# Optimization experiments

Hardware: AMD Instinct MI355X
Metric: run time of the kernel (lower is better)

Reference implementation:

```python
import jax, jax.numpy as jnp
import numpy as np

B, S, CC, CF, E, H, NH = 16, 1024, 8, 8, 64, 1024, 16
DH = H // NH
VOCAB = 10000
EPS = 1e-5


def layer_norm(x, g, b):
    m = x.mean(-1, keepdims=True)
    v = x.var(-1, keepdims=True)
    return (x - m) / jnp.sqrt(v + EPS) * g + b


def setup_inputs():
    key = jax.random.key(0)
    ks = jax.random.split(key, 30)
    f32 = jnp.float32
    n = lambda k, shp, s=0.02: jax.random.normal(k, shp, f32) * s
    inp = {}
    inp['cate_x'] = jax.random.randint(ks[0], (B, S, CC), 0, VOCAB)
    inp['cont_x'] = jax.random.normal(ks[1], (B, S, CF), f32)
    inp['mask'] = jax.random.randint(ks[2], (B, S), 0, 2)
    # parameters
    inp['emb_table'] = n(ks[3], (VOCAB, E)).at[0].set(0.0)  # padding_idx=0
    inp['cate_W'] = n(ks[4], (CC * E, H)); inp['cate_b'] = jnp.zeros((H,), f32)
    inp['cate_ln_g'] = jnp.ones((H,), f32); inp['cate_ln_b'] = jnp.zeros((H,), f32)
    inp['bn_g'] = jnp.ones((CF,), f32); inp['bn_b'] = jnp.zeros((CF,), f32)
    inp['cont_W'] = n(ks[5], (CF, H)); inp['cont_b'] = jnp.zeros((H,), f32)
    inp['cont_ln_g'] = jnp.ones((H,), f32); inp['cont_ln_b'] = jnp.zeros((H,), f32)
    inp['comb_W'] = n(ks[6], (2 * H, H)); inp['comb_b'] = jnp.zeros((H,), f32)
    inp['comb_ln_g'] = jnp.ones((H,), f32); inp['comb_ln_b'] = jnp.zeros((H,), f32)
    inp['Wq'] = n(ks[7], (H, H)); inp['bq'] = jnp.zeros((H,), f32)
    inp['Wk'] = n(ks[8], (H, H)); inp['bk'] = jnp.zeros((H,), f32)
    inp['Wv'] = n(ks[9], (H, H)); inp['bv'] = jnp.zeros((H,), f32)
    inp['Wo'] = n(ks[10], (H, H)); inp['bo'] = jnp.zeros((H,), f32)
    return inp


def reference(cate_x, cont_x, mask, emb_table, cate_W, cate_b, cate_ln_g, cate_ln_b,
              bn_g, bn_b, cont_W, cont_b, cont_ln_g, cont_ln_b,
              comb_W, comb_b, comb_ln_g, comb_ln_b,
              Wq, bq, Wk, bk, Wv, bv, Wo, bo):
    # categorical path: embed -> flatten cols -> Linear+LN
    cate_emb = emb_table[cate_x].reshape(B, S, CC * E)
    cate_h = layer_norm(cate_emb @ cate_W + cate_b, cate_ln_g, cate_ln_b)
    # continuous path: BatchNorm1d over flattened (B*S, CF) with batch stats
    xf = cont_x.reshape(-1, CF)
    mu = xf.mean(0)
    var = xf.var(0)  # biased, as torch BN normalization
    xn = ((xf - mu) / jnp.sqrt(var + EPS) * bn_g + bn_b).reshape(B, S, CF)
    cont_h = layer_norm(xn @ cont_W + cont_b, cont_ln_g, cont_ln_b)
    # combine: ReLU -> Linear -> LN
    seq = jax.nn.relu(jnp.concatenate([cate_h, cont_h], axis=2))
    x = layer_norm(seq @ comb_W + comb_b, comb_ln_g, comb_ln_b)  # [B,S,H]
    # multi-head attention (dropout is identity in eval)
    Q = (x @ Wq + bq).reshape(B, S, NH, DH)
    K = (x @ Wk + bk).reshape(B, S, NH, DH)
    V = (x @ Wv + bv).reshape(B, S, NH, DH)
    scores = jnp.einsum('bqhd,bkhd->bhqk', Q, K) / np.sqrt(DH).astype(np.float32)
    # faithful to source: mask broadcast over the QUERY axis
    scores = jnp.where(mask[:, None, :, None] == 0, -1e7, scores)
    attn = jax.nn.softmax(scores, axis=-1)
    out = jnp.einsum('bhqk,bkhd->bqhd', attn, V).reshape(B, S, H)
    out = out @ Wo + bo
    return out[:, -1:, -1]  # [B,1]
```

## Files before the change

### kernel.cpp

```cpp
#include <hip/hip_runtime.h>
#include <hip/hip_bf16.h>
#include <math.h>

#define EPS 1e-5f

typedef unsigned short u16;
typedef __attribute__((ext_vector_type(8))) short bf16x8;
typedef __attribute__((ext_vector_type(4))) float f32x4;

__device__ __forceinline__ float b2f(u16 u) {
  union { unsigned int i; float f; } v; v.i = ((unsigned int)u) << 16; return v.f;
}
__device__ __forceinline__ u16 f2b(float f) {
  union { float f; unsigned int i; } v; v.f = f;
  unsigned int r = v.i + 0x7fff + ((v.i >> 16) & 1);
  return (u16)(r >> 16);
}

__device__ __forceinline__ void gload_lds16(const u16* g, u16* l) {
  __builtin_amdgcn_global_load_lds(
      (const __attribute__((address_space(1))) unsigned int*)g,
      (__attribute__((address_space(3))) unsigned int*)l, 16, 0, 0);
}

__global__ __launch_bounds__(256) void prep_k(
    const float* __restrict__ cx, float* __restrict__ part_bn,
    float* __restrict__ outacc,
    const float* __restrict__ emb, u16* __restrict__ embb,
    const float* __restrict__ cate_W, u16* __restrict__ cateWT,
    const float* __restrict__ comb_W, u16* __restrict__ combWT,
    const float* __restrict__ Wv, const float* __restrict__ Wo,
    float* __restrict__ wvo) {
  __shared__ float shmem[64 * 65];
  const int bid = blockIdx.x, tid = threadIdx.x;

  if (bid == 0) {
    if (tid < 16) outacc[tid] = 0.f;
    return;
  }
  if (bid <= 64) {
    int pb = bid - 1;
    int gid = pb * 256 + tid;
    float4 a = ((const float4*)cx)[2 * gid];
    float4 b = ((const float4*)cx)[2 * gid + 1];
    float v[16];
    v[0] = a.x; v[1] = a.y; v[2] = a.z; v[3] = a.w;
    v[4] = b.x; v[5] = b.y; v[6] = b.z; v[7] = b.w;
#pragma unroll
    for (int i = 0; i < 8; ++i) v[8 + i] = v[i] * v[i];
#pragma unroll
    for (int off = 32; off; off >>= 1)
#pragma unroll
      for (int i = 0; i < 16; ++i) v[i] += __shfl_down(v[i], off);
    int l = tid & 63, wv_ = tid >> 6;
    if (l == 0)
#pragma unroll
      for (int i = 0; i < 16; ++i) shmem[wv_ * 16 + i] = v[i];
    __syncthreads();
    if (tid < 16)
      part_bn[pb * 16 + tid] = shmem[tid] + shmem[16 + tid] + shmem[32 + tid] + shmem[48 + tid];
    return;
  }
  if (bid <= 689) {
    int i = (bid - 65) * 256 + tid;
    if (i < 160000) {
      float4 v = ((const float4*)emb)[i];
      ushort4 u; u.x = f2b(v.x); u.y = f2b(v.y); u.z = f2b(v.z); u.w = f2b(v.w);
      ((ushort4*)embb)[i] = u;
    }
    return;
  }
  if (bid <= 1329) {
    const float* W; u16* WT; int K, local;
    if (bid <= 817) { W = cate_W; WT = cateWT; K = 512;  local = bid - 690; }
    else            { W = comb_W; WT = combWT; K = 2048; local = bid - 818; }
    int n0 = (local & 15) * 64, k0 = (local >> 4) * 64;
    int c = tid & 63, r0 = tid >> 6;
#pragma unroll
    for (int i = 0; i < 16; ++i) {
      int r = r0 + i * 4;
      shmem[r * 65 + c] = W[(size_t)(k0 + r) * 1024 + n0 + c];
    }
    __syncthreads();
#pragma unroll
    for (int i = 0; i < 16; ++i) {
      int r = r0 + i * 4;
      WT[(size_t)(n0 + r) * K + k0 + c] = f2b(shmem[c * 65 + r]);
    }
    return;
  }
  {
    int local = bid - 1330;
    int h = local >> 2, jc = local & 3;
    if (tid < 64) shmem[tid] = Wo[(size_t)(h * 64 + tid) * 1024 + 1023];
    __syncthreads();
    int j = jc * 256 + tid;
    const float* vr = Wv + (size_t)j * 1024 + h * 64;
    float s = 0.f;
    for (int d4 = 0; d4 < 64; d4 += 4) {
      float4 w4 = *(const float4*)(vr + d4);
      s = fmaf(w4.x, shmem[d4], s);
      s = fmaf(w4.y, shmem[d4 + 1], s);
      s = fmaf(w4.z, shmem[d4 + 2], s);
      s = fmaf(w4.w, shmem[d4 + 3], s);
    }
    wvo[h * 1024 + j] = s;
  }
}

template <int MODE>
__global__ __launch_bounds__(512) void gemm256(
    const u16* __restrict__ A0, const u16* __restrict__ A1,
    const int* __restrict__ idx, const u16* __restrict__ embb,
    const u16* __restrict__ BT, const float* __restrict__ bias,
    u16* __restrict__ C, int K) {
  __shared__ u16 As[2][2][8192];
  __shared__ u16 Bs[2][2][8192];
  const int tid = threadIdx.x;
  const int bid = blockIdx.x;
  const int chunk = gridDim.x >> 3;
  const int swz = (bid & 7) * chunk + (bid >> 3);
  const int row0 = (swz >> 2) * 256;
  const int col0 = (swz & 3) * 256;

  const int rr8 = tid >> 3;
  const int p8  = tid & 7;
  const int sl  = p8 ^ (rr8 & 7);

  const int l   = tid & 63;
  const int w   = tid >> 6;
  const int wrh = w >> 2;
  const int wcq = w & 3;
  const int hb  = wcq >> 1;
  const int rbb = (wcq & 1) * 64;
  const int lr  = l & 15;
  const int lk  = l >> 4;

  f32x4 acc[8][4];
#pragma unroll
  for (int m = 0; m < 8; ++m)
#pragma unroll
    for (int n = 0; n < 4; ++n) acc[m][n] = (f32x4){0.f, 0.f, 0.f, 0.f};

  const int nt = K >> 6;
  const int nit = nt >> 1;

  auto stageA = [&](int t, int h) {
    const int k0 = t << 6;
    const int buf = t & 1;
#pragma unroll
    for (int i = 0; i < 2; ++i) {
      int ar = row0 + h * 128 + i * 64 + rr8;
      const u16* asrc;
      if (MODE == 1) {
        int id = idx[ar * 8 + (k0 >> 6)];
        asrc = embb + (size_t)id * 64 + sl * 8;
      } else {
        const u16* base = (k0 < 1024) ? A0 : A1;
        asrc = base + (size_t)ar * 1024 + (k0 & 1023) + sl * 8;
      }
      gload_lds16(asrc, &As[buf][h][i * 4096 + tid * 8]);
    }
  };
  auto stageB = [&](int t, int h) {
    const int k0 = t << 6;
    const int buf = t & 1;
#pragma unroll
    for (int i = 0; i < 2; ++i) {
      int br = col0 + h * 128 + i * 64 + rr8;
      gload_lds16(BT + (size_t)br * K + k0 + sl * 8,
                  &Bs[buf][h][i * 4096 + tid * 8]);
    }
  };

  bf16x8 bfr[4][2];
  auto loadB = [&](int buf) {
#pragma unroll
    for (int n = 0; n < 4; ++n)
#pragma unroll
      for (int ks = 0; ks < 2; ++ks) {
        int rowb = rbb + n * 16 + lr;
        int ph = (ks * 4 + lk) ^ (lr & 7);
        bfr[n][ks] = *(const bf16x8*)&Bs[buf][hb][rowb * 64 + ph * 8];
      }
  };
  auto loadA = [&](bf16x8 (&af)[2][2], int buf, int q) {
#pragma unroll
    for (int mm = 0; mm < 2; ++mm)
#pragma unroll
      for (int ks = 0; ks < 2; ++ks) {
        int rowa = (q * 2 + mm) * 16 + lr;
        int ph = (ks * 4 + lk) ^ (lr & 7);
        af[mm][ks] = *(const bf16x8*)&As[buf][wrh][rowa * 64 + ph * 8];
      }
  };
  auto mfma_quad = [&](bf16x8 (&af)[2][2], int q) {
    __builtin_amdgcn_s_setprio(1);
#pragma unroll
    for (int ks = 0; ks < 2; ++ks)
#pragma unroll
      for (int mm = 0; mm < 2; ++mm)
#pragma unroll
        for (int n = 0; n < 4; ++n)
          acc[q * 2 + mm][n] = __builtin_amdgcn_mfma_f32_16x16x32_bf16(
              af[mm][ks], bfr[n][ks], acc[q * 2 + mm][n], 0, 0, 0);
    __builtin_amdgcn_s_setprio(0);
  };

  stageA(0, 0); stageA(0, 1);
  stageB(0, 0); stageB(0, 1);
  stageB(1, 0); stageB(1, 1);
  asm volatile("s_waitcnt vmcnt(4)" ::: "memory");
  __builtin_amdgcn_s_barrier();

  for (int it = 0; it < nit; ++it) {
    const int T = it * 2;
    const bool more = (T + 2 < nt);
    bf16x8 af[2][2];

    loadB(0); loadA(af, 0, 0);
    stageA(T + 1, 0);
    __builtin_amdgcn_s_barrier();
    asm volatile("s_waitcnt lgkmcnt(0)" ::: "memory");
    mfma_quad(af, 0);
    __builtin_amdgcn_s_barrier();
    loadA(af, 0, 1);
    stageA(T + 1, 1);
    __builtin_amdgcn_s_barrier();
    asm volatile("s_waitcnt lgkmcnt(0)" ::: "memory");
    mfma_quad(af, 1);
    __builtin_amdgcn_s_barrier();
    loadA(af, 0, 2);
    if (more) stageB(T + 2, 0);
    __builtin_amdgcn_s_barrier();
    asm volatile("s_waitcnt lgkmcnt(0)" ::: "memory");
    mfma_quad(af, 2);
    __builtin_amdgcn_s_barrier();
    loadA(af, 0, 3);
    if (more) stageB(T + 2, 1);
    __builtin_amdgcn_s_barrier();
    asm volatile("s_waitcnt lgkmcnt(0)" ::: "memory");
    mfma_quad(af, 3);
    if (more) asm volatile("s_waitcnt vmcnt(4)" ::: "memory");
    else      asm volatile("s_waitcnt vmcnt(0)" ::: "memory");
    __builtin_amdgcn_s_barrier();

    loadB(1); loadA(af, 1, 0);
    if (more) stageA(T + 2, 0);
    __builtin_amdgcn_s_barrier();
    asm volatile("s_waitcnt lgkmcnt(0)" ::: "memory");
    mfma_quad(af, 0);
    __builtin_amdgcn_s_barrier();
    loadA(af, 1, 1);
    if (more) stageA(T + 2, 1);
    __builtin_amdgcn_s_barrier();
    asm volatile("s_waitcnt lgkmcnt(0)" ::: "memory");
    mfma_quad(af, 1);
    __builtin_amdgcn_s_barrier();
    loadA(af, 1, 2);
    if (more) stageB(T + 3, 0);
    __builtin_amdgcn_s_barrier();
    asm volatile("s_waitcnt lgkmcnt(0)" ::: "memory");
    mfma_quad(af, 2);
    __builtin_amdgcn_s_barrier();
    loadA(af, 1, 3);
    if (more) stageB(T + 3, 1);
    __builtin_amdgcn_s_barrier();
    asm volatile("s_waitcnt lgkmcnt(0)" ::: "memory");
    mfma_quad(af, 3);
    if (it + 1 < nit) {
      asm volatile("s_waitcnt vmcnt(4)" ::: "memory");
      __builtin_amdgcn_s_barrier();
    }
  }

  float bv_[4];
#pragma unroll
  for (int n = 0; n < 4; ++n) bv_[n] = bias[col0 + wcq * 64 + n * 16 + lr];
#pragma unroll
  for (int m = 0; m < 8; ++m) {
#pragma unroll
    for (int n = 0; n < 4; ++n) {
      int cc = col0 + wcq * 64 + n * 16 + lr;
#pragma unroll
      for (int q4 = 0; q4 < 4; ++q4) {
        int rr = row0 + wrh * 128 + m * 16 + lk * 4 + q4;
        C[(size_t)rr * 1024 + cc] = f2b(acc[m][n][q4] + bv_[n]);
      }
    }
  }
}

__global__ __launch_bounds__(256) void ln_k(u16* __restrict__ buf,
                                            const float* __restrict__ g,
                                            const float* __restrict__ b, int relu) {
  int lane = threadIdx.x & 63, wave = threadIdx.x >> 6;
  size_t row = (size_t)blockIdx.x * 4 + wave;
  u16* p = buf + row * 1024 + lane * 16;
  uint4 u0 = *(uint4*)p;
  uint4 u1 = *(uint4*)(p + 8);
  float x[16];
#pragma unroll
  for (int i = 0; i < 4; ++i) {
    unsigned int w0 = ((unsigned int*)&u0)[i];
    unsigned int w1 = ((unsigned int*)&u1)[i];
    x[2 * i]     = b2f((u16)(w0 & 0xffff));
    x[2 * i + 1] = b2f((u16)(w0 >> 16));
    x[8 + 2 * i]     = b2f((u16)(w1 & 0xffff));
    x[8 + 2 * i + 1] = b2f((u16)(w1 >> 16));
  }
  float s = 0.f, s2 = 0.f;
#pragma unroll
  for (int i = 0; i < 16; ++i) { s += x[i]; s2 += x[i] * x[i]; }
#pragma unroll
  for (int off = 32; off; off >>= 1) { s += __shfl_xor(s, off); s2 += __shfl_xor(s2, off); }
  float mean = s * (1.f / 1024.f);
  float var = s2 * (1.f / 1024.f) - mean * mean;
  float rs = rsqrtf(var + EPS);
  float y[16];
#pragma unroll
  for (int q = 0; q < 4; ++q) {
    float4 gv = *(const float4*)(g + lane * 16 + q * 4);
    float4 bv = *(const float4*)(b + lane * 16 + q * 4);
    y[4 * q]     = (x[4 * q]     - mean) * rs * gv.x + bv.x;
    y[4 * q + 1] = (x[4 * q + 1] - mean) * rs * gv.y + bv.y;
    y[4 * q + 2] = (x[4 * q + 2] - mean) * rs * gv.z + bv.z;
    y[4 * q + 3] = (x[4 * q + 3] - mean) * rs * gv.w + bv.w;
  }
  if (relu)
#pragma unroll
    for (int i = 0; i < 16; ++i) y[i] = fmaxf(y[i], 0.f);
  uint4 o0, o1;
#pragma unroll
  for (int i = 0; i < 4; ++i) {
    ((unsigned int*)&o0)[i] = (unsigned int)f2b(y[2 * i]) | ((unsigned int)f2b(y[2 * i + 1]) << 16);
    ((unsigned int*)&o1)[i] = (unsigned int)f2b(y[8 + 2 * i]) | ((unsigned int)f2b(y[8 + 2 * i + 1]) << 16);
  }
  *(uint4*)p = o0;
  *(uint4*)(p + 8) = o1;
}

__global__ __launch_bounds__(256) void cont_k(const float* __restrict__ cx,
                                              const float* __restrict__ part_bn,
                                              const float* __restrict__ bn_g,
                                              const float* __restrict__ bn_b,
                                              const float* __restrict__ W,
                                              const float* __restrict__ cb,
                                              const float* __restrict__ g,
                                              const float* __restrict__ bb,
                                              u16* __restrict__ out) {
  int row0 = blockIdx.x * 8, tid = threadIdx.x;
  __shared__ float sp[4][16];
  __shared__ float tt[16];
  __shared__ float ab[2][8];
  __shared__ float xn[8][8];
  __shared__ float rr1[4][8], rr2[4][8];

  if (tid < 64) {
    int f = tid & 15, qd = tid >> 4;
    float s = 0.f;
    for (int j = qd * 16; j < qd * 16 + 16; ++j) s += part_bn[j * 16 + f];
    sp[qd][f] = s;
  }
  __syncthreads();
  if (tid < 16) tt[tid] = sp[0][tid] + sp[1][tid] + sp[2][tid] + sp[3][tid];
  __syncthreads();
  if (tid < 8) {
    float mu = tt[tid] * (1.f / 16384.f);
    float var = tt[8 + tid] * (1.f / 16384.f) - mu * mu;
    float a = rsqrtf(var + EPS) * bn_g[tid];
    ab[0][tid] = a;
    ab[1][tid] = bn_b[tid] - mu * a;
  }
  __syncthreads();
  if (tid < 64) {
    int r = tid >> 3, f = tid & 7;
    xn[r][f] = ab[0][f] * cx[(row0 + r) * 8 + f] + ab[1][f];
  }
  __syncthreads();

  int c = tid * 4;
  float4 cbv = *(const float4*)(cb + c);
  float acc[8][4];
#pragma unroll
  for (int r = 0; r < 8; ++r) {
    acc[r][0] = cbv.x; acc[r][1] = cbv.y; acc[r][2] = cbv.z; acc[r][3] = cbv.w;
  }
  for (int k = 0; k < 8; ++k) {
    float4 w4 = *(const float4*)(W + k * 1024 + c);
#pragma unroll
    for (int r = 0; r < 8; ++r) {
      float xv = xn[r][k];
      acc[r][0] = fmaf(xv, w4.x, acc[r][0]);
      acc[r][1] = fmaf(xv, w4.y, acc[r][1]);
      acc[r][2] = fmaf(xv, w4.z, acc[r][2]);
      acc[r][3] = fmaf(xv, w4.w, acc[r][3]);
    }
  }
  float s1[8], s2[8];
#pragma unroll
  for (int r = 0; r < 8; ++r) {
    s1[r] = acc[r][0] + acc[r][1] + acc[r][2] + acc[r][3];
    s2[r] = acc[r][0] * acc[r][0] + acc[r][1] * acc[r][1] +
            acc[r][2] * acc[r][2] + acc[r][3] * acc[r][3];
  }
#pragma unroll
  for (int off = 32; off; off >>= 1)
#pragma unroll
    for (int r = 0; r < 8; ++r) {
      s1[r] += __shfl_down(s1[r], off);
      s2[r] += __shfl_down(s2[r], off);
    }
  int lane = tid & 63, wv = tid >> 6;
  if (lane == 0)
#pragma unroll
    for (int r = 0; r < 8; ++r) { rr1[wv][r] = s1[r]; rr2[wv][r] = s2[r]; }
  __syncthreads();
  float4 gv = *(const float4*)(g + c);
  float4 bv = *(const float4*)(bb + c);
#pragma unroll
  for (int r = 0; r < 8; ++r) {
    float ss = rr1[0][r] + rr1[1][r] + rr1[2][r] + rr1[3][r];
    float qq = rr2[0][r] + rr2[1][r] + rr2[2][r] + rr2[3][r];
    float mean = ss * (1.f / 1024.f);
    float var = qq * (1.f / 1024.f) - mean * mean;
    float rs = rsqrtf(var + EPS);
    float y0 = fmaxf((acc[r][0] - mean) * rs * gv.x + bv.x, 0.f);
    float y1 = fmaxf((acc[r][1] - mean) * rs * gv.y + bv.y, 0.f);
    float y2 = fmaxf((acc[r][2] - mean) * rs * gv.z + bv.z, 0.f);
    float y3 = fmaxf((acc[r][3] - mean) * rs * gv.w + bv.w, 0.f);
    ushort4 o; o.x = f2b(y0); o.y = f2b(y1); o.z = f2b(y2); o.w = f2b(y3);
    *(ushort4*)(out + (size_t)(row0 + r) * 1024 + c) = o;
  }
}

__global__ __launch_bounds__(256) void qproj_k(const u16* __restrict__ x,
                                               const float* __restrict__ Wq,
                                               const float* __restrict__ bq,
                                               float* __restrict__ q) {
  __shared__ u16 xs[16][1024];
  __shared__ float part[16][16][16];
  int tid = threadIdx.x;
  for (int i = tid; i < 4096; i += 256) {
    int b = i >> 8, off = (i & 255) * 4;
    *(ushort4*)&xs[b][off] =
        *(const ushort4*)(x + ((size_t)(b * 1024 + 1023)) * 1024 + off);
  }
  __syncthreads();
  int c = tid & 15;
  int col = blockIdx.x * 16 + c;
  int kq = tid >> 4;
  float acc[16];
#pragma unroll
  for (int b = 0; b < 16; ++b) acc[b] = 0.f;
  for (int k = kq * 64; k < kq * 64 + 64; ++k) {
    float wv = Wq[(size_t)k * 1024 + col];
#pragma unroll
    for (int b = 0; b < 16; ++b) acc[b] = fmaf(b2f(xs[b][k]), wv, acc[b]);
  }
#pragma unroll
  for (int b = 0; b < 16; ++b) part[kq][b][c] = acc[b];
  __syncthreads();
  if (tid < 256) {
    int b = tid >> 4, cc = tid & 15;
    float s = 0.f;
#pragma unroll
    for (int j = 0; j < 16; ++j) s += part[j][b][cc];
    q[b * 1024 + blockIdx.x * 16 + cc] = s + bq[blockIdx.x * 16 + cc];
  }
}

__global__ __launch_bounds__(256) void kq_k(const float* __restrict__ Wk,
                                            const float* __restrict__ bk,
                                            const float* __restrict__ q,
                                            u16* __restrict__ qtb,
                                            float* __restrict__ bkq) {
  int h = blockIdx.x >> 2, jc = blockIdx.x & 3;
  int tid = threadIdx.x;
  __shared__ float Qs[16][64];
  for (int i = tid; i < 1024; i += 256) {
    int b = i >> 6, d = i & 63;
    Qs[b][d] = q[b * 1024 + h * 64 + d];
  }
  __syncthreads();
  int j = jc * 256 + tid;
  float acc[16];
#pragma unroll
  for (int b = 0; b < 16; ++b) acc[b] = 0.f;
  const float* wr = Wk + (size_t)j * 1024 + h * 64;
  for (int d4 = 0; d4 < 64; d4 += 4) {
    float4 w4 = *(const float4*)(wr + d4);
#pragma unroll
    for (int b = 0; b < 16; ++b) {
      acc[b] = fmaf(w4.x, Qs[b][d4], acc[b]);
      acc[b] = fmaf(w4.y, Qs[b][d4 + 1], acc[b]);
      acc[b] = fmaf(w4.z, Qs[b][d4 + 2], acc[b]);
      acc[b] = fmaf(w4.w, Qs[b][d4 + 3], acc[b]);
    }
  }
#pragma unroll
  for (int b = 0; b < 16; ++b) qtb[((size_t)b * 16 + h) * 1024 + j] = f2b(acc[b]);
  if (jc == 0 && tid < 16) {
    int b = tid;
    float s = 0.f;
    for (int d = 0; d < 64; ++d) s = fmaf(bk[h * 64 + d], Qs[b][d], s);
    bkq[b * 16 + h] = s;
  }
}

__global__ __launch_bounds__(256) void score_k(const u16* __restrict__ x,
                                               const u16* __restrict__ qtb,
                                               const float* __restrict__ bkq,
                                               const int* __restrict__ mask,
                                               float* __restrict__ sc) {
  int b = blockIdx.x >> 4, kc = blockIdx.x & 15;
  int tid = threadIdx.x;
  int l = tid & 63, w = tid >> 6;
  int keybase = kc * 64 + w * 16;
  int lr = l & 15, ls = l >> 4;
  int masked = (mask[b * 1024 + 1023] == 0);

  f32x4 acc = (f32x4){0.f, 0.f, 0.f, 0.f};
  const u16* xb = x + (size_t)b * 1024 * 1024;
  const u16* qb = qtb + (size_t)b * 16 * 1024;
  for (int k0 = 0; k0 < 1024; k0 += 32) {
    bf16x8 bfr = *(const bf16x8*)&qb[(size_t)lr * 1024 + k0 + ls * 8];
    bf16x8 afr = *(const bf16x8*)&xb[(size_t)(keybase + lr) * 1024 + k0 + ls * 8];
    acc = __builtin_amdgcn_mfma_f32_16x16x32_bf16(afr, bfr, acc, 0, 0, 0);
  }
  int h = lr;
  float bq_ = bkq[b * 16 + h];
#pragma unroll
  for (int q = 0; q < 4; ++q) {
    int key = keybase + ls * 4 + q;
    float v = masked ? 0.f : (acc[q] + bq_) * 0.125f;
    sc[((size_t)b * 16 + h) * 1024 + key] = v;
  }
}

__global__ __launch_bounds__(256) void attnw_k(float* __restrict__ sc) {
  int bh = blockIdx.x, tid = threadIdx.x;
  float* row = sc + (size_t)bh * 1024;
  float4 v = ((float4*)row)[tid];
  float m = fmaxf(fmaxf(v.x, v.y), fmaxf(v.z, v.w));
#pragma unroll
  for (int off = 32; off; off >>= 1) m = fmaxf(m, __shfl_down(m, off));
  __shared__ float rm[4], rs_[4];
  int lane = tid & 63, wv = tid >> 6;
  if (lane == 0) rm[wv] = m;
  __syncthreads();
  m = fmaxf(fmaxf(rm[0], rm[1]), fmaxf(rm[2], rm[3]));
  float e0 = expf(v.x - m), e1 = expf(v.y - m), e2 = expf(v.z - m), e3 = expf(v.w - m);
  float s = e0 + e1 + e2 + e3;
#pragma unroll
  for (int off = 32; off; off >>= 1) s += __shfl_down(s, off);
  if (lane == 0) rs_[wv] = s;
  __syncthreads();
  s = rs_[0] + rs_[1] + rs_[2] + rs_[3];
  float inv = 1.f / s;
  float4 o; o.x = e0 * inv; o.y = e1 * inv; o.z = e2 * inv; o.w = e3 * inv;
  ((float4*)row)[tid] = o;
}

__global__ __launch_bounds__(256) void ctx_k(const float* __restrict__ p,
                                             const u16* __restrict__ x,
                                             const float* __restrict__ wvo,
                                             float* __restrict__ outacc) {
  int b = blockIdx.x >> 4, kc = blockIdx.x & 15;
  int tid = threadIdx.x;
  __shared__ float pl[64][16];
  for (int i = tid; i < 1024; i += 256) {
    int kk = i >> 4, hh = i & 15;
    pl[kk][hh] = p[((size_t)b * 16 + hh) * 1024 + kc * 64 + kk];
  }
  __syncthreads();
  float acc[16][4];
#pragma unroll
  for (int h = 0; h < 16; ++h)
#pragma unroll
    for (int j = 0; j < 4; ++j) acc[h][j] = 0.f;
  const u16* xb = x + ((size_t)(b * 1024 + kc * 64)) * 1024 + tid * 4;
  for (int k = 0; k < 64; ++k) {
    ushort4 u = *(const ushort4*)(xb + (size_t)k * 1024);
    float x0 = b2f(u.x), x1 = b2f(u.y), x2 = b2f(u.z), x3 = b2f(u.w);
#pragma unroll
    for (int h4 = 0; h4 < 4; ++h4) {
      float4 pv = *(const float4*)&pl[k][h4 * 4];
      acc[h4 * 4 + 0][0] = fmaf(pv.x, x0, acc[h4 * 4 + 0][0]);
      acc[h4 * 4 + 0][1] = fmaf(pv.x, x1, acc[h4 * 4 + 0][1]);
      acc[h4 * 4 + 0][2] = fmaf(pv.x, x2, acc[h4 * 4 + 0][2]);
      acc[h4 * 4 + 0][3] = fmaf(pv.x, x3, acc[h4 * 4 + 0][3]);
      acc[h4 * 4 + 1][0] = fmaf(pv.y, x0, acc[h4 * 4 + 1][0]);
      acc[h4 * 4 + 1][1] = fmaf(pv.y, x1, acc[h4 * 4 + 1][1]);
      acc[h4 * 4 + 1][2] = fmaf(pv.y, x2, acc[h4 * 4 + 1][2]);
      acc[h4 * 4 + 1][3] = fmaf(pv.y, x3, acc[h4 * 4 + 1][3]);
      acc[h4 * 4 + 2][0] = fmaf(pv.z, x0, acc[h4 * 4 + 2][0]);
      acc[h4 * 4 + 2][1] = fmaf(pv.z, x1, acc[h4 * 4 + 2][1]);
      acc[h4 * 4 + 2][2] = fmaf(pv.z, x2, acc[h4 * 4 + 2][2]);
      acc[h4 * 4 + 2][3] = fmaf(pv.z, x3, acc[h4 * 4 + 2][3]);
      acc[h4 * 4 + 3][0] = fmaf(pv.w, x0, acc[h4 * 4 + 3][0]);
      acc[h4 * 4 + 3][1] = fmaf(pv.w, x1, acc[h4 * 4 + 3][1]);
      acc[h4 * 4 + 3][2] = fmaf(pv.w, x2, acc[h4 * 4 + 3][2]);
      acc[h4 * 4 + 3][3] = fmaf(pv.w, x3, acc[h4 * 4 + 3][3]);
    }
  }
  float s = 0.f;
#pragma unroll
  for (int h = 0; h < 16; ++h) {
    float4 w4 = *(const float4*)&wvo[h * 1024 + tid * 4];
    s += acc[h][0] * w4.x + acc[h][1] * w4.y + acc[h][2] * w4.z + acc[h][3] * w4.w;
  }
#pragma unroll
  for (int off = 32; off; off >>= 1) s += __shfl_down(s, off);
  __shared__ float r[4];
  int lane = tid & 63, wv = tid >> 6;
  if (lane == 0) r[wv] = s;
  __syncthreads();
  if (tid == 0) atomicAdd(&outacc[b], r[0] + r[1] + r[2] + r[3]);
}

__global__ __launch_bounds__(256) void bfinal_k(const float* __restrict__ outacc,
                                                const float* __restrict__ bv,
                                                const float* __restrict__ Wo,
                                                const float* __restrict__ bo,
                                                float* __restrict__ out) {
  int tid = threadIdx.x;
  float s = 0.f;
  for (int i = tid; i < 1024; i += 256) s = fmaf(bv[i], Wo[(size_t)i * 1024 + 1023], s);
#pragma unroll
  for (int off = 32; off; off >>= 1) s += __shfl_down(s, off);
  __shared__ float r[4];
  int lane = tid & 63, wv = tid >> 6;
  if (lane == 0) r[wv] = s;
  __syncthreads();
  float bc = r[0] + r[1] + r[2] + r[3] + bo[1023];
  if (tid < 16) out[tid] = outacc[tid] + bc;
}

extern "C" void kernel_launch(void* const* d_in, const int* in_sizes, int n_in,
                              void* d_out, int out_size, void* d_ws, size_t ws_size,
                              hipStream_t stream) {
  const int*   cate_x  = (const int*)d_in[0];
  const float* cont_x  = (const float*)d_in[1];
  const int*   mask    = (const int*)d_in[2];
  const float* emb     = (const float*)d_in[3];
  const float* cate_W  = (const float*)d_in[4];
  const float* cate_b  = (const float*)d_in[5];
  const float* cate_g  = (const float*)d_in[6];
  const float* cate_bb = (const float*)d_in[7];
  const float* bn_g    = (const float*)d_in[8];
  const float* bn_b    = (const float*)d_in[9];
  const float* cont_W  = (const float*)d_in[10];
  const float* cont_b  = (const float*)d_in[11];
  const float* cont_g  = (const float*)d_in[12];
  const float* cont_bb = (const float*)d_in[13];
  const float* Wq = (const float*)d_in[18]; const float* bq = (const float*)d_in[19];
  const float* Wk = (const float*)d_in[20]; const float* bk = (const float*)d_in[21];
  const float* Wv = (const float*)d_in[22]; const float* bv = (const float*)d_in[23];
  const float* Wo = (const float*)d_in[24]; const float* bo = (const float*)d_in[25];
  const float* comb_W  = (const float*)d_in[14];
  const float* comb_b  = (const float*)d_in[15];
  const float* comb_g  = (const float*)d_in[16];
  const float* comb_bb = (const float*)d_in[17];
  float* out = (float*)d_out;

  char* w = (char*)d_ws;
  float* stats   = (float*)w;
  float* outacc  = stats + 16;
  float* part_bn = (float*)(w + 256);
  float* qbuf    = (float*)(w + 8192);
  u16* embb      = (u16*)(w + 131328);
  u16* cateWT    = (u16*)(w + 1411328);
  u16* combWT    = (u16*)(w + 2459904);
  float* sc      = (float*)(w + 6654208);
  u16*   qtb     = (u16*)(w + 7702784);
  float* wvo     = (float*)(w + 8227072);
  float* bkq     = (float*)(w + 8292608);
  u16* X1        = (u16*)(w + 10848512);
  u16* X2        = X1 + (size_t)16777216;
  u16* xb        = X2 + (size_t)16777216;

  prep_k<<<1394, 256, 0, stream>>>(cont_x, part_bn, outacc, emb, embb,
                                   cate_W, cateWT, comb_W, combWT, Wv, Wo, wvo);

  gemm256<1><<<256, 512, 0, stream>>>(nullptr, nullptr, cate_x, embb, cateWT,
                                      cate_b, X1, 512);
  ln_k<<<4096, 256, 0, stream>>>(X1, cate_g, cate_bb, 1);
  cont_k<<<2048, 256, 0, stream>>>(cont_x, part_bn, bn_g, bn_b, cont_W, cont_b,
                                   cont_g, cont_bb, X2);
  gemm256<2><<<256, 512, 0, stream>>>(X1, X2, nullptr, nullptr, combWT,
                                      comb_b, xb, 2048);
  ln_k<<<4096, 256, 0, stream>>>(xb, comb_g, comb_bb, 0);

  qproj_k<<<64, 256, 0, stream>>>(xb, Wq, bq, qbuf);
  kq_k<<<64, 256, 0, stream>>>(Wk, bk, qbuf, qtb, bkq);
  score_k<<<256, 256, 0, stream>>>(xb, qtb, bkq, mask, sc);
  attnw_k<<<256, 256, 0, stream>>>(sc);
  ctx_k<<<256, 256, 0, stream>>>(sc, xb, wvo, outacc);
  bfinal_k<<<1, 256, 0, stream>>>(outacc, bv, Wo, bo, out);
}
```

Before: 210.1 us.

## Merge LN, cont path and weight prep into one mid kernel; stage gather indices in LDS

The comb_W transpose and the Wv·Wo precompute move out of the prep kernel. They are fused with the categorical LayerNorm and the continuous-path kernel into a single heterogeneous launch that runs after the first GEMM. This trims the prep kernel ahead of the first GEMM and removes one launch. The embedding GEMM now preloads its gather indices into shared memory instead of reading them from global memory per stage, and the block-to-tile swizzle is changed. The mixed-role kernel carries extra LDS per block, and branch-divergent roles may schedule unevenly.

```diff
diff --git a/kernel.cpp b/kernel.cpp
--- a/kernel.cpp
+++ b/kernel.cpp
@@ -27,10 +27,7 @@
     const float* __restrict__ cx, float* __restrict__ part_bn,
     float* __restrict__ outacc,
     const float* __restrict__ emb, u16* __restrict__ embb,
-    const float* __restrict__ cate_W, u16* __restrict__ cateWT,
-    const float* __restrict__ comb_W, u16* __restrict__ combWT,
-    const float* __restrict__ Wv, const float* __restrict__ Wo,
-    float* __restrict__ wvo) {
+    const float* __restrict__ cate_W, u16* __restrict__ cateWT) {
   __shared__ float shmem[64 * 65];
   const int bid = blockIdx.x, tid = threadIdx.x;
 
@@ -70,27 +67,397 @@
     }
     return;
   }
-  if (bid <= 1329) {
-    const float* W; u16* WT; int K, local;
-    if (bid <= 817) { W = cate_W; WT = cateWT; K = 512;  local = bid - 690; }
-    else            { W = comb_W; WT = combWT; K = 2048; local = bid - 818; }
+  {
+    int local = bid - 690;
     int n0 = (local & 15) * 64, k0 = (local >> 4) * 64;
     int c = tid & 63, r0 = tid >> 6;
 #pragma unroll
     for (int i = 0; i < 16; ++i) {
       int r = r0 + i * 4;
-      shmem[r * 65 + c] = W[(size_t)(k0 + r) * 1024 + n0 + c];
+      shmem[r * 65 + c] = cate_W[(size_t)(k0 + r) * 1024 + n0 + c];
     }
     __syncthreads();
 #pragma unroll
     for (int i = 0; i < 16; ++i) {
       int r = r0 + i * 4;
-      WT[(size_t)(n0 + r) * K + k0 + c] = f2b(shmem[c * 65 + r]);
-    }
+      cateWT[(size_t)(n0 + r) * 512 + k0 + c] = f2b(shmem[c * 65 + r]);
+    }
+  }
+}
+
+template <int MODE>
+__global__ __launch_bounds__(512) void gemm256(
+    const u16* __restrict__ A0, const u16* __restrict__ A1,
+    const int* __restrict__ idx, const u16* __restrict__ embb,
+    const u16* __restrict__ BT, const float* __restrict__ bias,
+    u16* __restrict__ C, int K) {
+  __shared__ u16 As[2][2][8192];
+  __shared__ u16 Bs[2][2][8192];
+  __shared__ int sidx[MODE == 1 ? 2048 : 4];
+  const int tid = threadIdx.x;
+  const int bid = blockIdx.x;
+  const int col0 = (bid & 3) * 256;
+  const int row0 = ((((bid >> 2) & 1) << 5) + (bid >> 3)) * 256;
+
+  const int rr8 = tid >> 3;
+  const int p8  = tid & 7;
+  const int sl  = p8 ^ (rr8 & 7);
+
+  const int l   = tid & 63;
+  const int w   = tid >> 6;
+  const int wrh = w >> 2;
+  const int wcq = w & 3;
+  const int hb  = wcq >> 1;
+  const int rbb = (wcq & 1) * 64;
+  const int lr  = l & 15;
+  const int lk  = l >> 4;
+
+  f32x4 acc[8][4];
+#pragma unroll
+  for (int m = 0; m < 8; ++m)
+#pragma unroll
+    for (int n = 0; n < 4; ++n) acc[m][n] = (f32x4){0.f, 0.f, 0.f, 0.f};
+
+  const int nt = K >> 6;
+  const int nit = nt >> 1;
+
+  if (MODE == 1) {
+    *(int4*)&sidx[tid * 4] = *(const int4*)&idx[row0 * 8 + tid * 4];
+    __syncthreads();
+  }
+
+  auto stageA = [&](int t, int h) {
+    const int k0 = t << 6;
+    const int buf = t & 1;
+#pragma unroll
+    for (int i = 0; i < 2; ++i) {
+      const u16* asrc;
+      if (MODE == 1) {
+        int id = sidx[(h * 128 + i * 64 + rr8) * 8 + (k0 >> 6)];
+        asrc = embb + (size_t)id * 64 + sl * 8;
+      } else {
+        int ar = row0 + h * 128 + i * 64 + rr8;
+        const u16* base = (k0 < 1024) ? A0 : A1;
+        asrc = base + (size_t)ar * 1024 + (k0 & 1023) + sl * 8;
+      }
+      gload_lds16(asrc, &As[buf][h][i * 4096 + tid * 8]);
+    }
+  };
+  auto stageB = [&](int t, int h) {
+    const int k0 = t << 6;
+    const int buf = t & 1;
+#pragma unroll
+    for (int i = 0; i < 2; ++i) {
+      int br = col0 + h * 128 + i * 64 + rr8;
+      gload_lds16(BT + (size_t)br * K + k0 + sl * 8,
+                  &Bs[buf][h][i * 4096 + tid * 8]);
+    }
+  };
+
+  bf16x8 bfr[4][2];
+  auto loadB = [&](int buf) {
+#pragma unroll
+    for (int n = 0; n < 4; ++n)
+#pragma unroll
+      for (int ks = 0; ks < 2; ++ks) {
+        int rowb = rbb + n * 16 + lr;
+        int ph = (ks * 4 + lk) ^ (lr & 7);
+        bfr[n][ks] = *(const bf16x8*)&Bs[buf][hb][rowb * 64 + ph * 8];
+      }
+  };
+  auto loadA = [&](bf16x8 (&af)[2][2], int buf, int q) {
+#pragma unroll
+    for (int mm = 0; mm < 2; ++mm)
+#pragma unroll
+      for (int ks = 0; ks < 2; ++ks) {
+        int rowa = (q * 2 + mm) * 16 + lr;
+        int ph = (ks * 4 + lk) ^ (lr & 7);
+        af[mm][ks] = *(const bf16x8*)&As[buf][wrh][rowa * 64 + ph * 8];
+      }
+  };
+  auto mfma_quad = [&](bf16x8 (&af)[2][2], int q) {
+    __builtin_amdgcn_s_setprio(1);
+#pragma unroll
+    for (int ks = 0; ks < 2; ++ks)
+#pragma unroll
+      for (int mm = 0; mm < 2; ++mm)
+#pragma unroll
+        for (int n = 0; n < 4; ++n)
+          acc[q * 2 + mm][n] = __builtin_amdgcn_mfma_f32_16x16x32_bf16(
+              af[mm][ks], bfr[n][ks], acc[q * 2 + mm][n], 0, 0, 0);
+    __builtin_amdgcn_s_setprio(0);
+  };
+
+  stageA(0, 0); stageA(0, 1);
+  stageB(0, 0); stageB(0, 1);
+  stageB(1, 0); stageB(1, 1);
+  asm volatile("s_waitcnt vmcnt(4)" ::: "memory");
+  __builtin_amdgcn_s_barrier();
+
+  for (int it = 0; it < nit; ++it) {
+    const int T = it * 2;
+    const bool more = (T + 2 < nt);
+    bf16x8 af[2][2];
+
+    loadB(0); loadA(af, 0, 0);
+    stageA(T + 1, 0);
+    __builtin_amdgcn_s_barrier();
+    asm volatile("s_waitcnt lgkmcnt(0)" ::: "memory");
+    mfma_quad(af, 0);
+    __builtin_amdgcn_s_barrier();
+    loadA(af, 0, 1);
+    stageA(T + 1, 1);
+    __builtin_amdgcn_s_barrier();
+    asm volatile("s_waitcnt lgkmcnt(0)" ::: "memory");
+    mfma_quad(af, 1);
+    __builtin_amdgcn_s_barrier();
+    loadA(af, 0, 2);
+    if (more) stageB(T + 2, 0);
+    __builtin_amdgcn_s_barrier();
+    asm volatile("s_waitcnt lgkmcnt(0)" ::: "memory");
+    mfma_quad(af, 2);
+    __builtin_amdgcn_s_barrier();
+    loadA(af, 0, 3);
+    if (more) stageB(T + 2, 1);
+    __builtin_amdgcn_s_barrier();
+    asm volatile("s_waitcnt lgkmcnt(0)" ::: "memory");
+    mfma_quad(af, 3);
+    if (more) asm volatile("s_waitcnt vmcnt(4)" ::: "memory");
+    else      asm volatile("s_waitcnt vmcnt(0)" ::: "memory");
+    __builtin_amdgcn_s_barrier();
+
+    loadB(1); loadA(af, 1, 0);
+    if (more) stageA(T + 2, 0);
+    __builtin_amdgcn_s_barrier();
+    asm volatile("s_waitcnt lgkmcnt(0)" ::: "memory");
+    mfma_quad(af, 0);
+    __builtin_amdgcn_s_barrier();
+    loadA(af, 1, 1);
+    if (more) stageA(T + 2, 1);
+    __builtin_amdgcn_s_barrier();
+    asm volatile("s_waitcnt lgkmcnt(0)" ::: "memory");
+    mfma_quad(af, 1);
+    __builtin_amdgcn_s_barrier();
+    loadA(af, 1, 2);
+    if (more) stageB(T + 3, 0);
+    __builtin_amdgcn_s_barrier();
+    asm volatile("s_waitcnt lgkmcnt(0)" ::: "memory");
+    mfma_quad(af, 2);
+    __builtin_amdgcn_s_barrier();
+    loadA(af, 1, 3);
+    if (more) stageB(T + 3, 1);
+    __builtin_amdgcn_s_barrier();
+    asm volatile("s_waitcnt lgkmcnt(0)" ::: "memory");
+    mfma_quad(af, 3);
+    if (it + 1 < nit) {
+      asm volatile("s_waitcnt vmcnt(4)" ::: "memory");
+      __builtin_amdgcn_s_barrier();
+    }
+  }
+
+  float bv_[4];
+#pragma unroll
+  for (int n = 0; n < 4; ++n) bv_[n] = bias[col0 + wcq * 64 + n * 16 + lr];
+#pragma unroll
+  for (int m = 0; m < 8; ++m) {
+#pragma unroll
+    for (int n = 0; n < 4; ++n) {
+      int cc = col0 + wcq * 64 + n * 16 + lr;
+#pragma unroll
+      for (int q4 = 0; q4 < 4; ++q4) {
+        int rr = row0 + wrh * 128 + m * 16 + lk * 4 + q4;
+        C[(size_t)rr * 1024 + cc] = f2b(acc[m][n][q4] + bv_[n]);
+      }
+    }
+  }
+}
+
+__device__ __forceinline__ void ln_body(u16* __restrict__ buf,
+                                        const float* __restrict__ g,
+                                        const float* __restrict__ b, int relu,
+                                        int blk, int tid) {
+  int lane = tid & 63, wave = tid >> 6;
+  size_t row = (size_t)blk * 4 + wave;
+  u16* p = buf + row * 1024 + lane * 16;
+  uint4 u0 = *(uint4*)p;
+  uint4 u1 = *(uint4*)(p + 8);
+  float x[16];
+#pragma unroll
+  for (int i = 0; i < 4; ++i) {
+    unsigned int w0 = ((unsigned int*)&u0)[i];
+    unsigned int w1 = ((unsigned int*)&u1)[i];
+    x[2 * i]     = b2f((u16)(w0 & 0xffff));
+    x[2 * i + 1] = b2f((u16)(w0 >> 16));
+    x[8 + 2 * i]     = b2f((u16)(w1 & 0xffff));
+    x[8 + 2 * i + 1] = b2f((u16)(w1 >> 16));
+  }
+  float s = 0.f, s2 = 0.f;
+#pragma unroll
+  for (int i = 0; i < 16; ++i) { s += x[i]; s2 += x[i] * x[i]; }
+#pragma unroll
+  for (int off = 32; off; off >>= 1) { s += __shfl_xor(s, off); s2 += __shfl_xor(s2, off); }
+  float mean = s * (1.f / 1024.f);
+  float var = s2 * (1.f / 1024.f) - mean * mean;
+  float rs = rsqrtf(var + EPS);
+  float y[16];
+#pragma unroll
+  for (int q = 0; q < 4; ++q) {
+    float4 gv = *(const float4*)(g + lane * 16 + q * 4);
+    float4 bv = *(const float4*)(b + lane * 16 + q * 4);
+    y[4 * q]     = (x[4 * q]     - mean) * rs * gv.x + bv.x;
+    y[4 * q + 1] = (x[4 * q + 1] - mean) * rs * gv.y + bv.y;
+    y[4 * q + 2] = (x[4 * q + 2] - mean) * rs * gv.z + bv.z;
+    y[4 * q + 3] = (x[4 * q + 3] - mean) * rs * gv.w + bv.w;
+  }
+  if (relu)
+#pragma unroll
+    for (int i = 0; i < 16; ++i) y[i] = fmaxf(y[i], 0.f);
+  uint4 o0, o1;
+#pragma unroll
+  for (int i = 0; i < 4; ++i) {
+    ((unsigned int*)&o0)[i] = (unsigned int)f2b(y[2 * i]) | ((unsigned int)f2b(y[2 * i + 1]) << 16);
+    ((unsigned int*)&o1)[i] = (unsigned int)f2b(y[8 + 2 * i]) | ((unsigned int)f2b(y[8 + 2 * i + 1]) << 16);
+  }
+  *(uint4*)p = o0;
+  *(uint4*)(p + 8) = o1;
+}
+
+__global__ __launch_bounds__(256) void ln_k(u16* __restrict__ buf,
+                                            const float* __restrict__ g,
+                                            const float* __restrict__ b, int relu) {
+  ln_body(buf, g, b, relu, blockIdx.x, threadIdx.x);
+}
+
+__device__ __forceinline__ void cont_body(const float* __restrict__ cx,
+                                          const float* __restrict__ part_bn,
+                                          const float* __restrict__ bn_g,
+                                          const float* __restrict__ bn_b,
+                                          const float* __restrict__ W,
+                                          const float* __restrict__ cb,
+                                          const float* __restrict__ g,
+                                          const float* __restrict__ bb,
+                                          u16* __restrict__ out,
+                                          int row0, int tid) {
+  __shared__ float sp[4][16];
+  __shared__ float tt[16];
+  __shared__ float ab[2][8];
+  __shared__ float xn[8][8];
+  __shared__ float rr1[4][8], rr2[4][8];
+
+  if (tid < 64) {
+    int f = tid & 15, qd = tid >> 4;
+    float s = 0.f;
+    for (int j = qd * 16; j < qd * 16 + 16; ++j) s += part_bn[j * 16 + f];
+    sp[qd][f] = s;
+  }
+  __syncthreads();
+  if (tid < 16) tt[tid] = sp[0][tid] + sp[1][tid] + sp[2][tid] + sp[3][tid];
+  __syncthreads();
+  if (tid < 8) {
+    float mu = tt[tid] * (1.f / 16384.f);
+    float var = tt[8 + tid] * (1.f / 16384.f) - mu * mu;
+    float a = rsqrtf(var + EPS) * bn_g[tid];
+    ab[0][tid] = a;
+    ab[1][tid] = bn_b[tid] - mu * a;
+  }
+  __syncthreads();
+  if (tid < 64) {
+    int r = tid >> 3, f = tid & 7;
+    xn[r][f] = ab[0][f] * cx[(row0 + r) * 8 + f] + ab[1][f];
+  }
+  __syncthreads();
+
+  int c = tid * 4;
+  float4 cbv = *(const float4*)(cb + c);
+  float acc[8][4];
+#pragma unroll
+  for (int r = 0; r < 8; ++r) {
+    acc[r][0] = cbv.x; acc[r][1] = cbv.y; acc[r][2] = cbv.z; acc[r][3] = cbv.w;
+  }
+  for (int k = 0; k < 8; ++k) {
+    float4 w4 = *(const float4*)(W + k * 1024 + c);
+#pragma unroll
+    for (int r = 0; r < 8; ++r) {
+      float xv = xn[r][k];
+      acc[r][0] = fmaf(xv, w4.x, acc[r][0]);
+      acc[r][1] = fmaf(xv, w4.y, acc[r][1]);
+      acc[r][2] = fmaf(xv, w4.z, acc[r][2]);
+      acc[r][3] = fmaf(xv, w4.w, acc[r][3]);
+    }
+  }
+  float s1[8], s2[8];
+#pragma unroll
+  for (int r = 0; r < 8; ++r) {
+    s1[r] = acc[r][0] + acc[r][1] + acc[r][2] + acc[r][3];
+    s2[r] = acc[r][0] * acc[r][0] + acc[r][1] * acc[r][1] +
+            acc[r][2] * acc[r][2] + acc[r][3] * acc[r][3];
+  }
+#pragma unroll
+  for (int off = 32; off; off >>= 1)
+#pragma unroll
+    for (int r = 0; r < 8; ++r) {
+      s1[r] += __shfl_down(s1[r], off);
+      s2[r] += __shfl_down(s2[r], off);
+    }
+  int lane = tid & 63, wv = tid >> 6;
+  if (lane == 0)
+#pragma unroll
+    for (int r = 0; r < 8; ++r) { rr1[wv][r] = s1[r]; rr2[wv][r] = s2[r]; }
+  __syncthreads();
+  float4 gv = *(const float4*)(g + c);
+  float4 bv = *(const float4*)(bb + c);
+#pragma unroll
+  for (int r = 0; r < 8; ++r) {
+    float ss = rr1[0][r] + rr1[1][r] + rr1[2][r] + rr1[3][r];
+    float qq = rr2[0][r] + rr2[1][r] + rr2[2][r] + rr2[3][r];
+    float mean = ss * (1.f / 1024.f);
+    float var = qq * (1.f / 1024.f) - mean * mean;
+    float rs = rsqrtf(var + EPS);
+    float y0 = fmaxf((acc[r][0] - mean) * rs * gv.x + bv.x, 0.f);
+    float y1 = fmaxf((acc[r][1] - mean) * rs * gv.y + bv.y, 0.f);
+    float y2 = fmaxf((acc[r][2] - mean) * rs * gv.z + bv.z, 0.f);
+    float y3 = fmaxf((acc[r][3] - mean) * rs * gv.w + bv.w, 0.f);
+    ushort4 o; o.x = f2b(y0); o.y = f2b(y1); o.z = f2b(y2); o.w = f2b(y3);
+    *(ushort4*)(out + (size_t)(row0 + r) * 1024 + c) = o;
+  }
+}
+
+__global__ __launch_bounds__(256) void mid_k(
+    u16* __restrict__ X1, const float* __restrict__ cate_g,
+    const float* __restrict__ cate_bb,
+    const float* __restrict__ comb_W, u16* __restrict__ combWT,
+    const float* __restrict__ Wv, const float* __restrict__ Wo,
+    float* __restrict__ wvo,
+    const float* __restrict__ cx, const float* __restrict__ part_bn,
+    const float* __restrict__ bn_g, const float* __restrict__ bn_b,
+    const float* __restrict__ cont_W, const float* __restrict__ cont_b,
+    const float* __restrict__ cont_g, const float* __restrict__ cont_bb,
+    u16* __restrict__ X2) {
+  __shared__ float shmem[64 * 65];
+  const int bid = blockIdx.x, tid = threadIdx.x;
+  if (bid < 4096) {
+    ln_body(X1, cate_g, cate_bb, 1, bid, tid);
     return;
   }
-  {
-    int local = bid - 1330;
+  if (bid < 4608) {
+    int local = bid - 4096;
+    int n0 = (local & 15) * 64, k0 = (local >> 4) * 64;
+    int c = tid & 63, r0 = tid >> 6;
+#pragma unroll
+    for (int i = 0; i < 16; ++i) {
+      int r = r0 + i * 4;
+      shmem[r * 65 + c] = comb_W[(size_t)(k0 + r) * 1024 + n0 + c];
+    }
+    __syncthreads();
+#pragma unroll
+    for (int i = 0; i < 16; ++i) {
+      int r = r0 + i * 4;
+      combWT[(size_t)(n0 + r) * 2048 + k0 + c] = f2b(shmem[c * 65 + r]);
+    }
+    return;
+  }
+  if (bid < 4672) {
+    int local = bid - 4608;
     int h = local >> 2, jc = local & 3;
     if (tid < 64) shmem[tid] = Wo[(size_t)(h * 64 + tid) * 1024 + 1023];
     __syncthreads();
@@ -105,332 +472,12 @@
       s = fmaf(w4.w, shmem[d4 + 3], s);
     }
     wvo[h * 1024 + j] = s;
-  }
-}
-
-template <int MODE>
-__global__ __launch_bounds__(512) void gemm256(
-    const u16* __restrict__ A0, const u16* __restrict__ A1,
-    const int* __restrict__ idx, const u16* __restrict__ embb,
-    const u16* __restrict__ BT, const float* __restrict__ bias,
-    u16* __restrict__ C, int K) {
-  __shared__ u16 As[2][2][8192];
-  __shared__ u16 Bs[2][2][8192];
-  const int tid = threadIdx.x;
-  const int bid = blockIdx.x;
-  const int chunk = gridDim.x >> 3;
-  const int swz = (bid & 7) * chunk + (bid >> 3);
-  const int row0 = (swz >> 2) * 256;
-  const int col0 = (swz & 3) * 256;
-
-  const int rr8 = tid >> 3;
-  const int p8  = tid & 7;
-  const int sl  = p8 ^ (rr8 & 7);
-
-  const int l   = tid & 63;
-  const int w   = tid >> 6;
-  const int wrh = w >> 2;
-  const int wcq = w & 3;
-  const int hb  = wcq >> 1;
-  const int rbb = (wcq & 1) * 64;
-  const int lr  = l & 15;
-  const int lk  = l >> 4;
-
-  f32x4 acc[8][4];
-#pragma unroll
-  for (int m = 0; m < 8; ++m)
-#pragma unroll
-    for (int n = 0; n < 4; ++n) acc[m][n] = (f32x4){0.f, 0.f, 0.f, 0.f};
-
-  const int nt = K >> 6;
-  const int nit = nt >> 1;
-
-  auto stageA = [&](int t, int h) {
-    const int k0 = t << 6;
-    const int buf = t & 1;
-#pragma unroll
-    for (int i = 0; i < 2; ++i) {
-      int ar = row0 + h * 128 + i * 64 + rr8;
-      const u16* asrc;
-      if (MODE == 1) {
-        int id = idx[ar * 8 + (k0 >> 6)];
-        asrc = embb + (size_t)id * 64 + sl * 8;
-      } else {
-        const u16* base = (k0 < 1024) ? A0 : A1;
-        asrc = base + (size_t)ar * 1024 + (k0 & 1023) + sl * 8;
-      }
-      gload_lds16(asrc, &As[buf][h][i * 4096 + tid * 8]);
-    }
-  };
-  auto stageB = [&](int t, int h) {
-    const int k0 = t << 6;
-    const int buf = t & 1;
-#pragma unroll
-    for (int i = 0; i < 2; ++i) {
-      int br = col0 + h * 128 + i * 64 + rr8;
-      gload_lds16(BT + (size_t)br * K + k0 + sl * 8,
-                  &Bs[buf][h][i * 4096 + tid * 8]);
-    }
-  };
-
-  bf16x8 bfr[4][2];
-  auto loadB = [&](int buf) {
-#pragma unroll
-    for (int n = 0; n < 4; ++n)
-#pragma unroll
-      for (int ks = 0; ks < 2; ++ks) {
-        int rowb = rbb + n * 16 + lr;
-        int ph = (ks * 4 + lk) ^ (lr & 7);
-        bfr[n][ks] = *(const bf16x8*)&Bs[buf][hb][rowb * 64 + ph * 8];
-      }
-  };
-  auto loadA = [&](bf16x8 (&af)[2][2], int buf, int q) {
-#pragma unroll
-    for (int mm = 0; mm < 2; ++mm)
-#pragma unroll
-      for (int ks = 0; ks < 2; ++ks) {
-        int rowa = (q * 2 + mm) * 16 + lr;
-        int ph = (ks * 4 + lk) ^ (lr & 7);
-        af[mm][ks] = *(const bf16x8*)&As[buf][wrh][rowa * 64 + ph * 8];
-      }
-  };
-  auto mfma_quad = [&](bf16x8 (&af)[2][2], int q) {
-    __builtin_amdgcn_s_setprio(1);
-#pragma unroll
-    for (int ks = 0; ks < 2; ++ks)
-#pragma unroll
-      for (int mm = 0; mm < 2; ++mm)
-#pragma unroll
-        for (int n = 0; n < 4; ++n)
-          acc[q * 2 + mm][n] = __builtin_amdgcn_mfma_f32_16x16x32_bf16(
-              af[mm][ks], bfr[n][ks], acc[q * 2 + mm][n], 0, 0, 0);
-    __builtin_amdgcn_s_setprio(0);
-  };
-
-  stageA(0, 0); stageA(0, 1);
-  stageB(0, 0); stageB(0, 1);
-  stageB(1, 0); stageB(1, 1);
-  asm volatile("s_waitcnt vmcnt(4)" ::: "memory");
-  __builtin_amdgcn_s_barrier();
-
-  for (int it = 0; it < nit; ++it) {
-    const int T = it * 2;
-    const bool more = (T + 2 < nt);
-    bf16x8 af[2][2];
-
-    loadB(0); loadA(af, 0, 0);
-    stageA(T + 1, 0);
-    __builtin_amdgcn_s_barrier();
-    asm volatile("s_waitcnt lgkmcnt(0)" ::: "memory");
-    mfma_quad(af, 0);
-    __builtin_amdgcn_s_barrier();
-    loadA(af, 0, 1);
-    stageA(T + 1, 1);
-    __builtin_amdgcn_s_barrier();
-    asm volatile("s_waitcnt lgkmcnt(0)" ::: "memory");
-    mfma_quad(af, 1);
-    __builtin_amdgcn_s_barrier();
-    loadA(af, 0, 2);
-    if (more) stageB(T + 2, 0);
-    __builtin_amdgcn_s_barrier();
-    asm volatile("s_waitcnt lgkmcnt(0)" ::: "memory");
-    mfma_quad(af, 2);
-    __builtin_amdgcn_s_barrier();
-    loadA(af, 0, 3);
-    if (more) stageB(T + 2, 1);
-    __builtin_amdgcn_s_barrier();
-    asm volatile("s_waitcnt lgkmcnt(0)" ::: "memory");
-    mfma_quad(af, 3);
-    if (more) asm volatile("s_waitcnt vmcnt(4)" ::: "memory");
-    else      asm volatile("s_waitcnt vmcnt(0)" ::: "memory");
-    __builtin_amdgcn_s_barrier();
-
-    loadB(1); loadA(af, 1, 0);
-    if (more) stageA(T + 2, 0);
-    __builtin_amdgcn_s_barrier();
-    asm volatile("s_waitcnt lgkmcnt(0)" ::: "memory");
-    mfma_quad(af, 0);
-    __builtin_amdgcn_s_barrier();
-    loadA(af, 1, 1);
-    if (more) stageA(T + 2, 1);
-    __builtin_amdgcn_s_barrier();
-    asm volatile("s_waitcnt lgkmcnt(0)" ::: "memory");
-    mfma_quad(af, 1);
-    __builtin_amdgcn_s_barrier();
-    loadA(af, 1, 2);
-    if (more) stageB(T + 3, 0);
-    __builtin_amdgcn_s_barrier();
-    asm volatile("s_waitcnt lgkmcnt(0)" ::: "memory");
-    mfma_quad(af, 2);
-    __builtin_amdgcn_s_barrier();
-    loadA(af, 1, 3);
-    if (more) stageB(T + 3, 1);
-    __builtin_amdgcn_s_barrier();
-    asm volatile("s_waitcnt lgkmcnt(0)" ::: "memory");
-    mfma_quad(af, 3);
-    if (it + 1 < nit) {
-      asm volatile("s_waitcnt vmcnt(4)" ::: "memory");
-      __builtin_amdgcn_s_barrier();
-    }
-  }
-
-  float bv_[4];
-#pragma unroll
-  for (int n = 0; n < 4; ++n) bv_[n] = bias[col0 + wcq * 64 + n * 16 + lr];
-#pragma unroll
-  for (int m = 0; m < 8; ++m) {
-#pragma unroll
-    for (int n = 0; n < 4; ++n) {
-      int cc = col0 + wcq * 64 + n * 16 + lr;
-#pragma unroll
-      for (int q4 = 0; q4 < 4; ++q4) {
-        int rr = row0 + wrh * 128 + m * 16 + lk * 4 + q4;
-        C[(size_t)rr * 1024 + cc] = f2b(acc[m][n][q4] + bv_[n]);
-      }
-    }
-  }
-}
-
-__global__ __launch_bounds__(256) void ln_k(u16* __restrict__ buf,
-                                            const float* __restrict__ g,
-                                            const float* __restrict__ b, int relu) {
-  int lane = threadIdx.x & 63, wave = threadIdx.x >> 6;
-  size_t row = (size_t)blockIdx.x * 4 + wave;
-  u16* p = buf + row * 1024 + lane * 16;
-  uint4 u0 = *(uint4*)p;
-  uint4 u1 = *(uint4*)(p + 8);
-  float x[16];
-#pragma unroll
-  for (int i = 0; i < 4; ++i) {
-    unsigned int w0 = ((unsigned int*)&u0)[i];
-    unsigned int w1 = ((unsigned int*)&u1)[i];
-    x[2 * i]     = b2f((u16)(w0 & 0xffff));
-    x[2 * i + 1] = b2f((u16)(w0 >> 16));
-    x[8 + 2 * i]     = b2f((u16)(w1 & 0xffff));
-    x[8 + 2 * i + 1] = b2f((u16)(w1 >> 16));
-  }
-  float s = 0.f, s2 = 0.f;
-#pragma unroll
-  for (int i = 0; i < 16; ++i) { s += x[i]; s2 += x[i] * x[i]; }
-#pragma unroll
-  for (int off = 32; off; off >>= 1) { s += __shfl_xor(s, off); s2 += __shfl_xor(s2, off); }
-  float mean = s * (1.f / 1024.f);
-  float var = s2 * (1.f / 1024.f) - mean * mean;
-  float rs = rsqrtf(var + EPS);
-  float y[16];
-#pragma unroll
-  for (int q = 0; q < 4; ++q) {
-    float4 gv = *(const float4*)(g + lane * 16 + q * 4);
-    float4 bv = *(const float4*)(b + lane * 16 + q * 4);
-    y[4 * q]     = (x[4 * q]     - mean) * rs * gv.x + bv.x;
-    y[4 * q + 1] = (x[4 * q + 1] - mean) * rs * gv.y + bv.y;
-    y[4 * q + 2] = (x[4 * q + 2] - mean) * rs * gv.z + bv.z;
-    y[4 * q + 3] = (x[4 * q + 3] - mean) * rs * gv.w + bv.w;
-  }
-  if (relu)
-#pragma unroll
-    for (int i = 0; i < 16; ++i) y[i] = fmaxf(y[i], 0.f);
-  uint4 o0, o1;
-#pragma unroll
-  for (int i = 0; i < 4; ++i) {
-    ((unsigned int*)&o0)[i] = (unsigned int)f2b(y[2 * i]) | ((unsigned int)f2b(y[2 * i + 1]) << 16);
-    ((unsigned int*)&o1)[i] = (unsigned int)f2b(y[8 + 2 * i]) | ((unsigned int)f2b(y[8 + 2 * i + 1]) << 16);
-  }
-  *(uint4*)p = o0;
-  *(uint4*)(p + 8) = o1;
-}
-
-__global__ __launch_bounds__(256) void cont_k(const float* __restrict__ cx,
-                                              const float* __restrict__ part_bn,
-                                              const float* __restrict__ bn_g,
-                                              const float* __restrict__ bn_b,
-                                              const float* __restrict__ W,
-                                              const float* __restrict__ cb,
-                                              const float* __restrict__ g,
-                                              const float* __restrict__ bb,
-                                              u16* __restrict__ out) {
-  int row0 = blockIdx.x * 8, tid = threadIdx.x;
-  __shared__ float sp[4][16];
-  __shared__ float tt[16];
-  __shared__ float ab[2][8];
-  __shared__ float xn[8][8];
-  __shared__ float rr1[4][8], rr2[4][8];
-
-  if (tid < 64) {
-    int f = tid & 15, qd = tid >> 4;
-    float s = 0.f;
-    for (int j = qd * 16; j < qd * 16 + 16; ++j) s += part_bn[j * 16 + f];
-    sp[qd][f] = s;
-  }
-  __syncthreads();
-  if (tid < 16) tt[tid] = sp[0][tid] + sp[1][tid] + sp[2][tid] + sp[3][tid];
-  __syncthreads();
-  if (tid < 8) {
-    float mu = tt[tid] * (1.f / 16384.f);
-    float var = tt[8 + tid] * (1.f / 16384.f) - mu * mu;
-    float a = rsqrtf(var + EPS) * bn_g[tid];
-    ab[0][tid] = a;
-    ab[1][tid] = bn_b[tid] - mu * a;
-  }
-  __syncthreads();
-  if (tid < 64) {
-    int r = tid >> 3, f = tid & 7;
-    xn[r][f] = ab[0][f] * cx[(row0 + r) * 8 + f] + ab[1][f];
-  }
-  __syncthreads();
-
-  int c = tid * 4;
-  float4 cbv = *(const float4*)(cb + c);
-  float acc[8][4];
-#pragma unroll
-  for (int r = 0; r < 8; ++r) {
-    acc[r][0] = cbv.x; acc[r][1] = cbv.y; acc[r][2] = cbv.z; acc[r][3] = cbv.w;
-  }
-  for (int k = 0; k < 8; ++k) {
-    float4 w4 = *(const float4*)(W + k * 1024 + c);
-#pragma unroll
-    for (int r = 0; r < 8; ++r) {
-      float xv = xn[r][k];
-      acc[r][0] = fmaf(xv, w4.x, acc[r][0]);
-      acc[r][1] = fmaf(xv, w4.y, acc[r][1]);
-      acc[r][2] = fmaf(xv, w4.z, acc[r][2]);
-      acc[r][3] = fmaf(xv, w4.w, acc[r][3]);
-    }
-  }
-  float s1[8], s2[8];
-#pragma unroll
-  for (int r = 0; r < 8; ++r) {
-    s1[r] = acc[r][0] + acc[r][1] + acc[r][2] + acc[r][3];
-    s2[r] = acc[r][0] * acc[r][0] + acc[r][1] * acc[r][1] +
-            acc[r][2] * acc[r][2] + acc[r][3] * acc[r][3];
-  }
-#pragma unroll
-  for (int off = 32; off; off >>= 1)
-#pragma unroll
-    for (int r = 0; r < 8; ++r) {
-      s1[r] += __shfl_down(s1[r], off);
-      s2[r] += __shfl_down(s2[r], off);
-    }
-  int lane = tid & 63, wv = tid >> 6;
-  if (lane == 0)
-#pragma unroll
-    for (int r = 0; r < 8; ++r) { rr1[wv][r] = s1[r]; rr2[wv][r] = s2[r]; }
-  __syncthreads();
-  float4 gv = *(const float4*)(g + c);
-  float4 bv = *(const float4*)(bb + c);
-#pragma unroll
-  for (int r = 0; r < 8; ++r) {
-    float ss = rr1[0][r] + rr1[1][r] + rr1[2][r] + rr1[3][r];
-    float qq = rr2[0][r] + rr2[1][r] + rr2[2][r] + rr2[3][r];
-    float mean = ss * (1.f / 1024.f);
-    float var = qq * (1.f / 1024.f) - mean * mean;
-    float rs = rsqrtf(var + EPS);
-    float y0 = fmaxf((acc[r][0] - mean) * rs * gv.x + bv.x, 0.f);
-    float y1 = fmaxf((acc[r][1] - mean) * rs * gv.y + bv.y, 0.f);
-    float y2 = fmaxf((acc[r][2] - mean) * rs * gv.z + bv.z, 0.f);
-    float y3 = fmaxf((acc[r][3] - mean) * rs * gv.w + bv.w, 0.f);
-    ushort4 o; o.x = f2b(y0); o.y = f2b(y1); o.z = f2b(y2); o.w = f2b(y3);
-    *(ushort4*)(out + (size_t)(row0 + r) * 1024 + c) = o;
+    return;
+  }
+  {
+    int row0 = (bid - 4672) * 8;
+    cont_body(cx, part_bn, bn_g, bn_b, cont_W, cont_b, cont_g, cont_bb, X2,
+              row0, tid);
   }
 }
 
@@ -680,14 +727,14 @@
   u16* X2        = X1 + (size_t)16777216;
   u16* xb        = X2 + (size_t)16777216;
 
-  prep_k<<<1394, 256, 0, stream>>>(cont_x, part_bn, outacc, emb, embb,
-                                   cate_W, cateWT, comb_W, combWT, Wv, Wo, wvo);
+  prep_k<<<818, 256, 0, stream>>>(cont_x, part_bn, outacc, emb, embb,
+                                  cate_W, cateWT);
 
   gemm256<1><<<256, 512, 0, stream>>>(nullptr, nullptr, cate_x, embb, cateWT,
                                       cate_b, X1, 512);
-  ln_k<<<4096, 256, 0, stream>>>(X1, cate_g, cate_bb, 1);
-  cont_k<<<2048, 256, 0, stream>>>(cont_x, part_bn, bn_g, bn_b, cont_W, cont_b,
-                                   cont_g, cont_bb, X2);
+  mid_k<<<6720, 256, 0, stream>>>(X1, cate_g, cate_bb, comb_W, combWT, Wv, Wo,
+                                  wvo, cont_x, part_bn, bn_g, bn_b, cont_W,
+                                  cont_b, cont_g, cont_bb, X2);
   gemm256<2><<<256, 512, 0, stream>>>(X1, X2, nullptr, nullptr, combWT,
                                       comb_b, xb, 2048);
   ln_k<<<4096, 256, 0, stream>>>(xb, comb_g, comb_bb, 0);
```

Result: no change. 213.8 us (+1.8%).
